# Performance work log

Measured on AMD Instinct MI355X. Metric: run time of the kernel, lower is better.

## Reference

```python
import jax, jax.numpy as jnp
import numpy as np

B, S, DV = 64, 200, 128
NC2, ND = 4096, 10000


def setup_inputs() -> dict:
    key = jax.random.key(0)
    ks = jax.random.split(key, 24)
    n = lambda k, shp: jax.random.normal(k, shp, dtype=jnp.float32) * 0.05
    return dict(
        c1_seq=jax.random.randint(ks[0], (B, S), 0, 1000),
        c2_seq=jax.random.randint(ks[1], (B, S), 0, NC2),
        c4_seq=jax.random.randint(ks[2], (B, S), 0, 1000),
        d_seq=jax.random.randint(ks[3], (B, S), 0, ND),
        r_seq=jax.random.randint(ks[4], (B, S), 0, 2),
        D_emb=n(ks[5], (ND, 1)),
        v_d=n(ks[6], (DV,)),
        v_c2=n(ks[7], (DV,)),
        R_emb=n(ks[8], (2, DV)),
        W_ih=n(ks[9], (3 * DV, 2 * DV)),
        W_hh=n(ks[10], (3 * DV, DV)),
        b_ih=n(ks[11], (3 * DV,)),
        b_hh=n(ks[12], (3 * DV,)),
        W1=n(ks[13], (DV, DV)), b1=n(ks[14], (DV,)),
        W2=n(ks[15], (1, DV)), b2=n(ks[16], (1,)),
        W3=n(ks[17], (DV, 3 * DV)), b3=n(ks[18], (DV,)),
        W4=n(ks[19], (1, DV)), b4=n(ks[20], (1,)),
    )


def reference(c1_seq, c2_seq, c4_seq, d_seq, r_seq, D_emb, v_d, v_c2, R_emb,
              W_ih, W_hh, b_ih, b_hh, W1, b1, W2, b2, W3, b3, W4, b4):
    # Dropout layers are identity in eval mode.
    gamma = D_emb[d_seq]                      # [B,S,1]
    v_d_seq = gamma * v_d                     # [B,S,DV]
    v_r_seq = R_emb[r_seq]                    # [B,S,DV]
    x = jnp.concatenate([v_d_seq, v_r_seq], axis=-1)  # [B,S,2DV]

    # torch-style GRU over time (batch_first). Precompute input projections.
    xW = jnp.einsum('bsi,gi->bsg', x, W_ih) + b_ih    # [B,S,3DV]

    def gru_step(h, xw_t):
        hW = h @ W_hh.T + b_hh
        xr, xz, xn = jnp.split(xw_t, 3, axis=-1)
        hr, hz, hn = jnp.split(hW, 3, axis=-1)
        r = jax.nn.sigmoid(xr + hr)
        z = jax.nn.sigmoid(xz + hz)
        n = jnp.tanh(xn + r * hn)
        h_new = (1.0 - z) * n + z * h
        return h_new, h_new

    h0 = jnp.zeros((B, DV), x.dtype)
    _, h_seq = jax.lax.scan(gru_step, h0, jnp.swapaxes(xW, 0, 1))
    h_seq = jnp.swapaxes(h_seq, 0, 1)         # [B,S,DV]

    alpha_seq = (jax.nn.relu(h_seq @ W1.T + b1) @ W2.T + b2)[..., 0]  # [B,S]

    rows = jnp.arange(B)

    def c2_step(C2, ts):
        c2_t, vd_t, vr_t = ts
        beta = jnp.take_along_axis(C2, c2_t[:, None], axis=-1)   # [B,1] gather
        v_c2_t = beta * v_c2                                     # [B,DV]
        feat = jnp.concatenate([v_c2_t, vd_t, vr_t], axis=-1)    # [B,3DV]
        new_c2 = (jax.nn.relu(feat @ W3.T + b3) @ W4.T + b4)[:, 0]
        # one-hot masked update == per-row scatter set
        C2 = C2.at[rows, c2_t].set(new_c2)
        return C2, C2

    C2_0 = jnp.zeros((B, NC2), x.dtype)
    _, C2_seq = jax.lax.scan(
        c2_step, C2_0,
        (jnp.swapaxes(c2_seq, 0, 1), jnp.swapaxes(v_d_seq, 0, 1), jnp.swapaxes(v_r_seq, 0, 1)))
    C2_seq = jnp.swapaxes(C2_seq, 0, 1)       # [B,S,NC2]

    return alpha_seq, h_seq, C2_seq
```

## Files before the change

### kernel.cpp

```cpp
#include <hip/hip_runtime.h>

namespace {
constexpr int B_ = 64, S_ = 200, DV_ = 128, NC2_ = 4096;
}

typedef float f4v __attribute__((ext_vector_type(4)));
typedef float f32x4 __attribute__((ext_vector_type(4)));
typedef _Float16 half8 __attribute__((ext_vector_type(8)));

__device__ __forceinline__ void lds_sync() {
  asm volatile("s_waitcnt lgkmcnt(0)\n\ts_barrier" ::: "memory");
}

__global__ __launch_bounds__(512, 1) void k1_gru_scanfill(
    const int* __restrict__ c2_seq, const int* __restrict__ d_seq,
    const int* __restrict__ r_seq, const float* __restrict__ D_emb,
    const float* __restrict__ v_d, const float* __restrict__ v_c2,
    const float* __restrict__ R_emb,
    const float* __restrict__ W_ih, const float* __restrict__ W_hh,
    const float* __restrict__ b_ih, const float* __restrict__ b_hh,
    const float* __restrict__ W3, const float* __restrict__ b3,
    const float* __restrict__ W4, const float* __restrict__ b4,
    float* __restrict__ out_h, float* __restrict__ out_c2)
{
  __shared__ __align__(16) char smem[18944];
  const int tid = threadIdx.x;

  if (blockIdx.x < B_) {
    const int b = blockIdx.x;
    _Float16* hist = reinterpret_cast<_Float16*>(smem);
    float* gl = reinterpret_cast<float*>(smem + 512);
    int* rl = reinterpret_cast<int*>(smem + 1312);
    float* u_l = reinterpret_cast<float*>(smem + 2112);
    float* p0_l = u_l + 384;
    float* p1_l = p0_l + 384;
    float* bh_l = p1_l + 384;

    for (int i = tid; i < S_; i += 512) {
      gl[i] = D_emb[d_seq[b * S_ + i]];
      rl[i] = r_seq[b * S_ + i];
    }
    if (tid < 256) reinterpret_cast<_Float16*>(hist)[tid] = (_Float16)0.f;

    if (tid < 384) {
      const int row = tid;
      const float4* wi =
          reinterpret_cast<const float4*>(W_ih + (size_t)row * 2 * DV_);
      const float4* vd4 = reinterpret_cast<const float4*>(v_d);
      const float4* re4 = reinterpret_cast<const float4*>(R_emb);
      float uu = 0.f, pp0 = 0.f, pp1 = 0.f;
#pragma unroll 8
      for (int k = 0; k < DV_ / 4; ++k) {
        float4 a = wi[k], vv = vd4[k];
        uu += a.x * vv.x + a.y * vv.y + a.z * vv.z + a.w * vv.w;
        float4 c = wi[DV_ / 4 + k];
        float4 r0 = re4[k], r1 = re4[DV_ / 4 + k];
        pp0 += c.x * r0.x + c.y * r0.y + c.z * r0.z + c.w * r0.w;
        pp1 += c.x * r1.x + c.y * r1.y + c.z * r1.z + c.w * r1.w;
      }
      const float bi = b_ih[row];
      u_l[row] = uu; p0_l[row] = pp0 + bi; p1_l[row] = pp1 + bi;
      bh_l[row] = b_hh[row];
    }

    const int w = tid >> 6, l = tid & 63;
    const int col = l & 15, kg = l >> 4;
    const int d = 16 * w + col;
    half8 bf[3][4];
#pragma unroll
    for (int g = 0; g < 3; ++g) {
      const float* wr = W_hh + (size_t)(g * DV_ + d) * DV_;
#pragma unroll
      for (int kt = 0; kt < 4; ++kt) {
        const int k0 = kt * 32 + kg * 8;
        const float4 lo = *reinterpret_cast<const float4*>(wr + k0);
        const float4 hi = *reinterpret_cast<const float4*>(wr + k0 + 4);
        half8 hb;
        hb[0] = (_Float16)lo.x; hb[1] = (_Float16)lo.y;
        hb[2] = (_Float16)lo.z; hb[3] = (_Float16)lo.w;
        hb[4] = (_Float16)hi.x; hb[5] = (_Float16)hi.y;
        hb[6] = (_Float16)hi.z; hb[7] = (_Float16)hi.w;
        bf[g][kt] = hb;
      }
    }
    __syncthreads();

    float u3[3], p03[3], p13[3], bh3[3];
#pragma unroll
    for (int g = 0; g < 3; ++g) {
      u3[g] = u_l[g * DV_ + d];
      p03[g] = p0_l[g * DV_ + d];
      p13[g] = p1_l[g * DV_ + d];
      bh3[g] = bh_l[g * DV_ + d];
    }
    float hprev = 0.f;
    float gv = gl[0];
    int rv = rl[0];

    float* outp = out_h + (size_t)b * S_ * DV_ + d;
    for (int t = 0; t < S_; ++t) {
      const int cur = t & 1;
      half8 af[4];
#pragma unroll
      for (int kt = 0; kt < 4; ++kt)
        af[kt] = *reinterpret_cast<const half8*>(&hist[cur * DV_ + kt * 32 + kg * 8]);
      f32x4 a0 = {0.f, 0.f, 0.f, 0.f}, a1 = a0, a2 = a0;
#pragma unroll
      for (int kt = 0; kt < 4; ++kt) {
        a0 = __builtin_amdgcn_mfma_f32_16x16x32_f16(af[kt], bf[0][kt], a0, 0, 0, 0);
        a1 = __builtin_amdgcn_mfma_f32_16x16x32_f16(af[kt], bf[1][kt], a1, 0, 0, 0);
        a2 = __builtin_amdgcn_mfma_f32_16x16x32_f16(af[kt], bf[2][kt], a2, 0, 0, 0);
      }
      const float xr = gv * u3[0] + (rv ? p13[0] : p03[0]);
      const float xz = gv * u3[1] + (rv ? p13[1] : p03[1]);
      const float xn = gv * u3[2] + (rv ? p13[2] : p03[2]);
      const float r = 1.f / (1.f + __expf(-(xr + a0[0] + bh3[0])));
      const float z = 1.f / (1.f + __expf(-(xz + a1[0] + bh3[1])));
      const float nx = xn + r * (a2[0] + bh3[2]);
      const float e2 = __expf(2.f * nx);
      const float n = (e2 - 1.f) / (e2 + 1.f);
      const float hnew = (1.f - z) * n + z * hprev;
      hprev = hnew;
      if (kg == 0) {
        outp[(size_t)t * DV_] = hnew;
        hist[(cur ^ 1) * DV_ + d] = (_Float16)hnew;
      }
      if (t + 1 < S_) { gv = gl[t + 1]; rv = rl[t + 1]; }
      lds_sync();
    }
  } else {
    const int b = blockIdx.x - B_;
    float* a3s = reinterpret_cast<float*>(smem);
    float* u3s = a3s + DV_;
    float* q0s = u3s + DV_;
    float* q1s = q0s + DV_;
    float* w4s = q1s + DV_;
    float* vals = w4s + DV_;
    float* gl = vals + S_;
    int* rl = reinterpret_cast<int*>(gl + S_);
    int* jl = rl + S_;
    int* prevs = jl + S_;
    int* done = prevs + S_;
    int* nresp = done + S_;

    if (tid == 0) *nresp = 0;
    for (int i = tid; i < S_; i += 512) {
      gl[i] = D_emb[d_seq[b * S_ + i]];
      rl[i] = r_seq[b * S_ + i];
      jl[i] = c2_seq[b * S_ + i];
      done[i] = 0;
    }
    if (tid < DV_) {
      const int d = tid;
      const float4* w3r = reinterpret_cast<const float4*>(W3 + (size_t)d * 3 * DV_);
      const float4* vc4 = reinterpret_cast<const float4*>(v_c2);
      const float4* vd4 = reinterpret_cast<const float4*>(v_d);
      const float4* re4 = reinterpret_cast<const float4*>(R_emb);
      float a3 = 0, u3 = 0, q0 = 0, q1 = 0;
#pragma unroll 8
      for (int k = 0; k < DV_ / 4; ++k) {
        float4 a = w3r[k], cc = vc4[k];
        a3 += a.x * cc.x + a.y * cc.y + a.z * cc.z + a.w * cc.w;
        float4 u = w3r[DV_ / 4 + k], dd = vd4[k];
        u3 += u.x * dd.x + u.y * dd.y + u.z * dd.z + u.w * dd.w;
        float4 cq = w3r[2 * (DV_ / 4) + k];
        float4 r0 = re4[k], r1 = re4[DV_ / 4 + k];
        q0 += cq.x * r0.x + cq.y * r0.y + cq.z * r0.z + cq.w * r0.w;
        q1 += cq.x * r1.x + cq.y * r1.y + cq.z * r1.z + cq.w * r1.w;
      }
      const float bb = b3[d];
      a3s[d] = a3; u3s[d] = u3; q0s[d] = q0 + bb; q1s[d] = q1 + bb;
      w4s[d] = W4[d];
    }
    __syncthreads();
    if (tid < S_) {
      const int jj = jl[tid];
      int p = -1;
      for (int q = tid - 1; q >= 0; --q)
        if (jl[q] == jj) { p = q; break; }
      prevs[tid] = p;
    }
    const float b4v = b4[0];
    __syncthreads();

    const int t = tid;
    const float gv = (t < S_) ? gl[t] : 0.f;
    const int rv = (t < S_) ? rl[t] : 0;
    const int p = (t < S_) ? prevs[t] : -1;
    bool mine_done = (t >= S_);

    for (int round = 0; round < S_; ++round) {
      float myval = 0.f;
      bool computed = false;
      if (!mine_done && (p < 0 || done[p])) {
        const float beta = (p < 0) ? 0.f : vals[p];
        const float4* a34 = reinterpret_cast<const float4*>(a3s);
        const float4* u34 = reinterpret_cast<const float4*>(u3s);
        const float4* q04 = reinterpret_cast<const float4*>(q0s);
        const float4* q14 = reinterpret_cast<const float4*>(q1s);
        const float4* w44 = reinterpret_cast<const float4*>(w4s);
        float acc = 0.f;
#pragma unroll 8
        for (int k = 0; k < DV_ / 4; ++k) {
          float4 a = a34[k], u = u34[k];
          float4 q = rv ? q14[k] : q04[k];
          float4 ww = w44[k];
          float h0 = beta * a.x + gv * u.x + q.x;
          float h1 = beta * a.y + gv * u.y + q.y;
          float h2 = beta * a.z + gv * u.z + q.z;
          float h3 = beta * a.w + gv * u.w + q.w;
          acc += ww.x * fmaxf(h0, 0.f) + ww.y * fmaxf(h1, 0.f) +
                 ww.z * fmaxf(h2, 0.f) + ww.w * fmaxf(h3, 0.f);
        }
        myval = acc + b4v;
        computed = true;
      }
      __syncthreads();
      if (computed) {
        vals[t] = myval;
        done[t] = 1;
        mine_done = true;
        atomicAdd(nresp, 1);
      }
      __syncthreads();
      if (*nresp >= S_) break;
    }
    __syncthreads();

    f4v v0 = {0.f, 0.f, 0.f, 0.f}, v1 = v0;
    f4v* dst4 = reinterpret_cast<f4v*>(out_c2 + (size_t)b * S_ * NC2_);
    for (int s = 0; s < S_; ++s) {
      const int j_ = jl[s];
      const int f_ = j_ >> 2;
      if ((f_ & 511) == tid) {
        const float vv_ = vals[s];
        const int rr_ = f_ >> 9, q_ = j_ & 3;
        if (rr_ == 0) {
          if (q_ == 0) v0.x = vv_; else if (q_ == 1) v0.y = vv_;
          else if (q_ == 2) v0.z = vv_; else v0.w = vv_;
        } else {
          if (q_ == 0) v1.x = vv_; else if (q_ == 1) v1.y = vv_;
          else if (q_ == 2) v1.z = vv_; else v1.w = vv_;
        }
      }
      f4v* drow = dst4 + (size_t)s * (NC2_ / 4);
      __builtin_nontemporal_store(v0, drow + tid);
      __builtin_nontemporal_store(v1, drow + tid + 512);
    }
  }
}

__global__ __launch_bounds__(256) void k2_alpha(
    const float* __restrict__ W1, const float* __restrict__ b1,
    const float* __restrict__ W2, const float* __restrict__ b2,
    const float* __restrict__ h_seq, float* __restrict__ out_alpha)
{
  const int tid = threadIdx.x;
  const int b = blockIdx.x >> 2, c = blockIdx.x & 3;
  const int sbeg = c * 50, send = sbeg + 50;
  __shared__ float4 hb4[2][DV_ / 4];
  __shared__ float red[4];
  const int grp = tid >> 7, d = tid & 127;
  float w1r[DV_];
  {
    const float4* wr = reinterpret_cast<const float4*>(W1 + (size_t)d * DV_);
#pragma unroll
    for (int k = 0; k < DV_ / 4; ++k) {
      float4 t4 = wr[k];
      w1r[4 * k] = t4.x; w1r[4 * k + 1] = t4.y;
      w1r[4 * k + 2] = t4.z; w1r[4 * k + 3] = t4.w;
    }
  }
  const float b1v = b1[d], w2v = W2[d], b2v = b2[0];
  float* hb = reinterpret_cast<float*>(hb4[grp]);
  for (int s = sbeg; s < send; s += 2) {
    const int ss = s + grp;
    hb[d] = h_seq[((size_t)(b * S_ + ss)) * DV_ + d];
    __syncthreads();
    float y0 = b1v, y1 = 0, y2 = 0, y3 = 0;
#pragma unroll
    for (int k = 0; k < DV_ / 4; ++k) {
      float4 hv = hb4[grp][k];
      y0 += w1r[4 * k + 0] * hv.x; y1 += w1r[4 * k + 1] * hv.y;
      y2 += w1r[4 * k + 2] * hv.z; y3 += w1r[4 * k + 3] * hv.w;
    }
    float part = w2v * fmaxf((y0 + y1) + (y2 + y3), 0.f);
#pragma unroll
    for (int off = 1; off < 64; off <<= 1) part += __shfl_xor(part, off);
    if ((tid & 63) == 0) red[tid >> 6] = part;
    __syncthreads();
    if (d == 0) out_alpha[b * S_ + ss] = red[2 * grp] + red[2 * grp + 1] + b2v;
    __syncthreads();
  }
}

extern "C" void kernel_launch(void* const* d_in, const int* in_sizes, int n_in,
                              void* d_out, int out_size, void* d_ws, size_t ws_size,
                              hipStream_t stream) {
  const int* c2_seq = (const int*)d_in[1];
  const int* d_seq = (const int*)d_in[3];
  const int* r_seq = (const int*)d_in[4];
  const float* D_emb = (const float*)d_in[5];
  const float* v_d = (const float*)d_in[6];
  const float* v_c2 = (const float*)d_in[7];
  const float* R_emb = (const float*)d_in[8];
  const float* W_ih = (const float*)d_in[9];
  const float* W_hh = (const float*)d_in[10];
  const float* b_ih = (const float*)d_in[11];
  const float* b_hh = (const float*)d_in[12];
  const float* W1 = (const float*)d_in[13];
  const float* b1 = (const float*)d_in[14];
  const float* W2 = (const float*)d_in[15];
  const float* b2 = (const float*)d_in[16];
  const float* W3 = (const float*)d_in[17];
  const float* b3 = (const float*)d_in[18];
  const float* W4 = (const float*)d_in[19];
  const float* b4 = (const float*)d_in[20];

  float* out = (float*)d_out;
  float* out_alpha = out;
  float* out_h = out + B_ * S_;
  float* out_c2 = out + B_ * S_ + (size_t)B_ * S_ * DV_;

  k1_gru_scanfill<<<dim3(2 * B_), dim3(512), 0, stream>>>(
      c2_seq, d_seq, r_seq, D_emb, v_d, v_c2, R_emb, W_ih, W_hh, b_ih, b_hh,
      W3, b3, W4, b4, out_h, out_c2);
  k2_alpha<<<dim3(256), dim3(256), 0, stream>>>(
      W1, b1, W2, b2, out_h, out_alpha);
}
```

Baseline: 155.2 us.

## Fuse alpha MLP into GRU blocks using LDS-resident fp16 history and MFMA

```diff
diff --git a/kernel.cpp b/kernel.cpp
--- a/kernel.cpp
+++ b/kernel.cpp
@@ -12,18 +12,21 @@
   asm volatile("s_waitcnt lgkmcnt(0)\n\ts_barrier" ::: "memory");
 }
 
-__global__ __launch_bounds__(512, 1) void k1_gru_scanfill(
+__global__ __launch_bounds__(512, 1) void k1_main(
     const int* __restrict__ c2_seq, const int* __restrict__ d_seq,
     const int* __restrict__ r_seq, const float* __restrict__ D_emb,
     const float* __restrict__ v_d, const float* __restrict__ v_c2,
     const float* __restrict__ R_emb,
     const float* __restrict__ W_ih, const float* __restrict__ W_hh,
     const float* __restrict__ b_ih, const float* __restrict__ b_hh,
+    const float* __restrict__ W1, const float* __restrict__ b1,
+    const float* __restrict__ W2, const float* __restrict__ b2,
     const float* __restrict__ W3, const float* __restrict__ b3,
     const float* __restrict__ W4, const float* __restrict__ b4,
-    float* __restrict__ out_h, float* __restrict__ out_c2)
+    float* __restrict__ out_alpha, float* __restrict__ out_h,
+    float* __restrict__ out_c2)
 {
-  __shared__ __align__(16) char smem[18944];
+  __shared__ __align__(16) char smem[18944 + 208 * DV_ * 2];
   const int tid = threadIdx.x;
 
   if (blockIdx.x < B_) {
@@ -35,12 +38,17 @@
     float* p0_l = u_l + 384;
     float* p1_l = p0_l + 384;
     float* bh_l = p1_l + 384;
+    _Float16* fullh = reinterpret_cast<_Float16*>(smem + 18944);
 
     for (int i = tid; i < S_; i += 512) {
       gl[i] = D_emb[d_seq[b * S_ + i]];
       rl[i] = r_seq[b * S_ + i];
     }
     if (tid < 256) reinterpret_cast<_Float16*>(hist)[tid] = (_Float16)0.f;
+    {
+      uint* fz = reinterpret_cast<uint*>(fullh + 200 * DV_);
+      for (int i = tid; i < 8 * DV_ / 2; i += 512) fz[i] = 0u;
+    }
 
     if (tid < 384) {
       const int row = tid;
@@ -123,11 +131,58 @@
       hprev = hnew;
       if (kg == 0) {
         outp[(size_t)t * DV_] = hnew;
-        hist[(cur ^ 1) * DV_ + d] = (_Float16)hnew;
+        const _Float16 hf = (_Float16)hnew;
+        hist[(cur ^ 1) * DV_ + d] = hf;
+        fullh[t * DV_ + (d ^ ((t & 7) << 3))] = hf;
       }
       if (t + 1 < S_) { gv = gl[t + 1]; rv = rl[t + 1]; }
       lds_sync();
     }
+
+    half8 bf1[4];
+    {
+      const float* wr1 = W1 + (size_t)d * DV_;
+#pragma unroll
+      for (int kt = 0; kt < 4; ++kt) {
+        const int k0 = kt * 32 + kg * 8;
+        const float4 lo = *reinterpret_cast<const float4*>(wr1 + k0);
+        const float4 hi = *reinterpret_cast<const float4*>(wr1 + k0 + 4);
+        half8 hb;
+        hb[0] = (_Float16)lo.x; hb[1] = (_Float16)lo.y;
+        hb[2] = (_Float16)lo.z; hb[3] = (_Float16)lo.w;
+        hb[4] = (_Float16)hi.x; hb[5] = (_Float16)hi.y;
+        hb[6] = (_Float16)hi.z; hb[7] = (_Float16)hi.w;
+        bf1[kt] = hb;
+      }
+    }
+    const float b1v = b1[d], w2v = W2[d], b2v = b2[0];
+    float* alphaAcc = u_l;
+    if (tid < 208) alphaAcc[tid] = b2v;
+    lds_sync();
+    for (int st = 0; st < 13; ++st) {
+      const int row = 16 * st + col;
+      half8 af2[4];
+#pragma unroll
+      for (int kt = 0; kt < 4; ++kt) {
+        const int c0 = (kt * 32 + kg * 8) ^ ((row & 7) << 3);
+        af2[kt] = *reinterpret_cast<const half8*>(&fullh[row * DV_ + c0]);
+      }
+      f32x4 y = {0.f, 0.f, 0.f, 0.f};
+#pragma unroll
+      for (int kt = 0; kt < 4; ++kt)
+        y = __builtin_amdgcn_mfma_f32_16x16x32_f16(af2[kt], bf1[kt], y, 0, 0, 0);
+#pragma unroll
+      for (int j = 0; j < 4; ++j) {
+        float part = w2v * fmaxf(y[j] + b1v, 0.f);
+        part += __shfl_xor(part, 1);
+        part += __shfl_xor(part, 2);
+        part += __shfl_xor(part, 4);
+        part += __shfl_xor(part, 8);
+        if (col == 0) atomicAdd(&alphaAcc[16 * st + 4 * kg + j], part);
+      }
+    }
+    lds_sync();
+    if (tid < S_) out_alpha[b * S_ + tid] = alphaAcc[tid];
   } else {
     const int b = blockIdx.x - B_;
     float* a3s = reinterpret_cast<float*>(smem);
@@ -250,50 +305,6 @@
   }
 }
 
-__global__ __launch_bounds__(256) void k2_alpha(
-    const float* __restrict__ W1, const float* __restrict__ b1,
-    const float* __restrict__ W2, const float* __restrict__ b2,
-    const float* __restrict__ h_seq, float* __restrict__ out_alpha)
-{
-  const int tid = threadIdx.x;
-  const int b = blockIdx.x >> 2, c = blockIdx.x & 3;
-  const int sbeg = c * 50, send = sbeg + 50;
-  __shared__ float4 hb4[2][DV_ / 4];
-  __shared__ float red[4];
-  const int grp = tid >> 7, d = tid & 127;
-  float w1r[DV_];
-  {
-    const float4* wr = reinterpret_cast<const float4*>(W1 + (size_t)d * DV_);
-#pragma unroll
-    for (int k = 0; k < DV_ / 4; ++k) {
-      float4 t4 = wr[k];
-      w1r[4 * k] = t4.x; w1r[4 * k + 1] = t4.y;
-      w1r[4 * k + 2] = t4.z; w1r[4 * k + 3] = t4.w;
-    }
-  }
-  const float b1v = b1[d], w2v = W2[d], b2v = b2[0];
-  float* hb = reinterpret_cast<float*>(hb4[grp]);
-  for (int s = sbeg; s < send; s += 2) {
-    const int ss = s + grp;
-    hb[d] = h_seq[((size_t)(b * S_ + ss)) * DV_ + d];
-    __syncthreads();
-    float y0 = b1v, y1 = 0, y2 = 0, y3 = 0;
-#pragma unroll
-    for (int k = 0; k < DV_ / 4; ++k) {
-      float4 hv = hb4[grp][k];
-      y0 += w1r[4 * k + 0] * hv.x; y1 += w1r[4 * k + 1] * hv.y;
-      y2 += w1r[4 * k + 2] * hv.z; y3 += w1r[4 * k + 3] * hv.w;
-    }
-    float part = w2v * fmaxf((y0 + y1) + (y2 + y3), 0.f);
-#pragma unroll
-    for (int off = 1; off < 64; off <<= 1) part += __shfl_xor(part, off);
-    if ((tid & 63) == 0) red[tid >> 6] = part;
-    __syncthreads();
-    if (d == 0) out_alpha[b * S_ + ss] = red[2 * grp] + red[2 * grp + 1] + b2v;
-    __syncthreads();
-  }
-}
-
 extern "C" void kernel_launch(void* const* d_in, const int* in_sizes, int n_in,
                               void* d_out, int out_size, void* d_ws, size_t ws_size,
                               hipStream_t stream) {
@@ -322,9 +333,7 @@
   float* out_h = out + B_ * S_;
   float* out_c2 = out + B_ * S_ + (size_t)B_ * S_ * DV_;
 
-  k1_gru_scanfill<<<dim3(2 * B_), dim3(512), 0, stream>>>(
+  k1_main<<<dim3(2 * B_), dim3(512), 0, stream>>>(
       c2_seq, d_seq, r_seq, D_emb, v_d, v_c2, R_emb, W_ih, W_hh, b_ih, b_hh,
-      W3, b3, W4, b4, out_h, out_c2);
-  k2_alpha<<<dim3(256), dim3(256), 0, stream>>>(
-      W1, b1, W2, b2, out_h, out_alpha);
+      W1, b1, W2, b2, W3, b3, W4, b4, out_alpha, out_h, out_c2);
 }
```

New measurement: 134.3 us, median of 2. 1.16x faster.
